# Performance work log

Measured on AMD Instinct MI355X. Metric: run time of the kernel, lower is better.

Reference implementation:

```python
import jax, jax.numpy as jnp
import numpy as np

ACT_BITS = 8
W_BITS = 8
BN_EPS = 1e-5


def _round_ste(x):
    # straight-through round (HAWQ-style ste_round)
    return x + jax.lax.stop_gradient(jnp.round(x) - x)


def _quant_sym(x, bits):
    # symmetric per-tensor fake quantization; scale treated as constant (EMA min/max in original)
    n = float(2 ** (bits - 1) - 1)
    s = jax.lax.stop_gradient(jnp.maximum(jnp.max(jnp.abs(x)) / n, 1e-8))
    xq = jnp.clip(_round_ste(x / s), -n - 1.0, n) * s
    return xq, s


def _conv(x, w, stride, pad):
    return jax.lax.conv_general_dilated(
        x, w, (stride, stride), [(pad, pad), (pad, pad)],
        dimension_numbers=("NCHW", "OIHW", "NCHW"))


def _quant_bn(x, gamma, beta, mean, var):
    # fold BN into a per-channel scale+bias; quantize the folded scale like a weight
    ws = gamma * jax.lax.rsqrt(var + BN_EPS)          # [C]
    wq, ws_scale = _quant_sym(ws, W_BITS)
    b = beta - mean * wq                               # [C]
    return x * wq[None, :, None, None] + b[None, :, None, None], ws_scale


def setup_inputs() -> dict:
    key = jax.random.key(0)
    ks = jax.random.split(key, 16)
    d = {}
    d["x"] = jax.random.normal(ks[0], (32, 128, 56, 56), jnp.float32)
    d["w1"] = jax.random.normal(ks[1], (256, 128, 3, 3), jnp.float32) * 0.05
    d["w2"] = jax.random.normal(ks[2], (256, 256, 3, 3), jnp.float32) * 0.05
    d["w_id"] = jax.random.normal(ks[3], (256, 128, 1, 1), jnp.float32) * 0.05
    for i, pfx in enumerate(["bn1", "bn2", "id"]):
        k4 = jax.random.split(ks[4 + i], 4)
        d[pfx + "_gamma"] = jax.random.uniform(k4[0], (256,), jnp.float32) + 0.5
        d[pfx + "_beta"] = jax.random.normal(k4[1], (256,), jnp.float32) * 0.1
        d[pfx + "_mean"] = jax.random.normal(k4[2], (256,), jnp.float32) * 0.1
        d[pfx + "_var"] = jax.random.uniform(k4[3], (256,), jnp.float32) + 0.5
    return d


def reference(x, w1, w2, w_id,
              bn1_gamma, bn1_beta, bn1_mean, bn1_var,
              bn2_gamma, bn2_beta, bn2_mean, bn2_var,
              id_gamma, id_beta, id_mean, id_var):
    # quant_act on block input
    xq, act_s = _quant_sym(x, ACT_BITS)

    # identity branch: 1x1 stride-2 quantized conv -> quant_act -> folded quant bn
    w_id_q, _ = _quant_sym(w_id, W_BITS)
    identity = _conv(xq, w_id_q, 2, 0)
    identity, _ = _quant_sym(identity, ACT_BITS)
    identity, _ = _quant_bn(identity, id_gamma, id_beta, id_mean, id_var)

    # main branch conv1 (3x3 stride 2) -> act quant -> bn -> relu -> act quant
    w1_q, _ = _quant_sym(w1, W_BITS)
    h = _conv(xq, w1_q, 2, 1)
    h, _ = _quant_sym(h, ACT_BITS)
    h, _ = _quant_bn(h, bn1_gamma, bn1_beta, bn1_mean, bn1_var)
    h = jax.nn.relu(h)
    h, _ = _quant_sym(h, ACT_BITS)

    # conv2 (3x3 stride 1) -> act quant -> bn
    w2_q, _ = _quant_sym(w2, W_BITS)
    h = _conv(h, w2_q, 1, 1)
    h, _ = _quant_sym(h, ACT_BITS)
    h, _ = _quant_bn(h, bn2_gamma, bn2_beta, bn2_mean, bn2_var)

    # residual add -> int32 requant -> relu
    h = h + identity
    h, out_s = _quant_sym(h, ACT_BITS)
    h = jax.nn.relu(h)
    return h, out_s
```

## Files before the change

### kernel.cpp

```cpp
#include <hip/hip_runtime.h>
#include <limits.h>

#define THREADS 256
#define GRID_BLOCKS 896

typedef int vi4 __attribute__((ext_vector_type(4)));

__device__ __forceinline__ float clamp8f(float q) { return fminf(fmaxf(q, -128.0f), 127.0f); }
__device__ __forceinline__ float sc_from_bits(unsigned b) {
  return fmaxf(__uint_as_float(b) / 127.0f, 1e-8f);
}
__device__ __forceinline__ signed char q8(float v, float s) {
  return (signed char)(int)clamp8f(rintf(v / s));
}


__device__ __forceinline__ void gbar(int* IS, int base, int bx) {
  asm volatile("s_waitcnt vmcnt(0)" ::: "memory");
  int old = __hip_atomic_fetch_add(IS + base + (bx & 7) * 16, 1, __ATOMIC_RELAXED,
                                   __HIP_MEMORY_SCOPE_AGENT);
  if (old == 111) {
    int r = __hip_atomic_fetch_add(IS + base + 128, 1, __ATOMIC_RELAXED, __HIP_MEMORY_SCOPE_AGENT);
    if (r == 7)
      __hip_atomic_fetch_add(IS + base + 144, 1, __ATOMIC_RELAXED, __HIP_MEMORY_SCOPE_AGENT);
  }
  while (__hip_atomic_load(IS + base + 144, __ATOMIC_RELAXED, __HIP_MEMORY_SCOPE_SYSTEM) == 0)
    __builtin_amdgcn_s_sleep(2);
}

__device__ __forceinline__ void amax_body(const float4* __restrict__ p, int n4, int bid,
                                          int nblocks, int* __restrict__ slot) {
  const int tid = threadIdx.x;
  const int stride = nblocks * THREADS;
  float m = 0.0f;
  int i = bid * THREADS + tid;
  for (; i + 3 * stride < n4; i += 4 * stride) {
    float4 v0 = p[i];
    float4 v1 = p[i + stride];
    float4 v2 = p[i + 2 * stride];
    float4 v3 = p[i + 3 * stride];
    float m0 = fmaxf(fmaxf(fabsf(v0.x), fabsf(v0.y)), fmaxf(fabsf(v0.z), fabsf(v0.w)));
    float m1 = fmaxf(fmaxf(fabsf(v1.x), fabsf(v1.y)), fmaxf(fabsf(v1.z), fabsf(v1.w)));
    float m2 = fmaxf(fmaxf(fabsf(v2.x), fabsf(v2.y)), fmaxf(fabsf(v2.z), fabsf(v2.w)));
    float m3 = fmaxf(fmaxf(fabsf(v3.x), fabsf(v3.y)), fmaxf(fabsf(v3.z), fabsf(v3.w)));
    m = fmaxf(m, fmaxf(fmaxf(m0, m1), fmaxf(m2, m3)));
  }
  for (; i < n4; i += stride) {
    float4 v = p[i];
    m = fmaxf(m, fmaxf(fmaxf(fabsf(v.x), fabsf(v.y)), fmaxf(fabsf(v.z), fabsf(v.w))));
  }
#pragma unroll
  for (int k = 32; k >= 1; k >>= 1) m = fmaxf(m, __shfl_xor(m, k));
  __shared__ float wred[4];
  if ((tid & 63) == 0) wred[tid >> 6] = m;
  __syncthreads();
  if (tid == 0) {
    m = fmaxf(fmaxf(wred[0], wred[1]), fmaxf(wred[2], wred[3]));
    atomicMax(slot, __float_as_int(m));
  }
}

__global__ __launch_bounds__(THREADS) void k_pre(
    int* IS, const float* g1, const float* be1, const float* m1, const float* v1, float* wq1,
    float* b1, const float* g2, const float* be2, const float* m2, const float* v2, float* wq2,
    float* b2, const float* gi, const float* bei, const float* mi, const float* vvi, float* wqi,
    float* bi, const float4* w1, const float4* w2, const float4* wid, const float4* x) {
  int b = blockIdx.x;
  int c = threadIdx.x;
  if (b < 3) {
    if (b == 0) {
      IS[128 + c] = 0;
      IS[384 + c] = 0;
      IS[640 + c] = 0;
      if (c < 192) IS[896 + c] = 0;
    }
    const float *gamma, *beta, *mean, *var;
    float *wq, *bb;
    if (b == 0) { gamma = g1; beta = be1; mean = m1; var = v1; wq = wq1; bb = b1; }
    else if (b == 1) { gamma = g2; beta = be2; mean = m2; var = v2; wq = wq2; bb = b2; }
    else { gamma = gi; beta = bei; mean = mi; var = vvi; wq = wqi; bb = bi; }
    __shared__ float red[THREADS];
    float ws = gamma[c] * (1.0f / sqrtf(var[c] + 1e-5f));
    red[c] = fabsf(ws);
    __syncthreads();
    for (int s = THREADS / 2; s > 0; s >>= 1) {
      if (c < s) red[c] = fmaxf(red[c], red[c + s]);
      __syncthreads();
    }
    float sws = fmaxf(red[0] / 127.0f, 1e-8f);
    float q = clamp8f(rintf(ws / sws)) * sws;
    wq[c] = q;
    bb[c] = beta[c] - mean[c] * q;
    return;
  }
  b -= 3;
  if (b < 64) { amax_body(w1, 73728, b, 64, IS + 1); return; }
  b -= 64;
  if (b < 128) { amax_body(w2, 147456, b, 128, IS + 2); return; }
  b -= 128;
  if (b < 16) { amax_body(wid, 8192, b, 16, IS + 3); return; }
  b -= 16;
  amax_body(x, 3211264, b, 512, IS + 0);
}

__global__ __launch_bounds__(THREADS) void k_quant(const float* __restrict__ x,
                                                   int* __restrict__ X8,
                                                   const float* __restrict__ w1f,
                                                   vi4* __restrict__ W1m,
                                                   const float* __restrict__ w2f,
                                                   vi4* __restrict__ W2m,
                                                   const float* __restrict__ widf,
                                                   vi4* __restrict__ Widm,
                                                   const unsigned* __restrict__ ISu) {
  __shared__ signed char tile[56 * 132];
  int b = blockIdx.x;
  int t = threadIdx.x;
  if (b < 1792) {
    float s = sc_from_bits(ISu[0]);
    int h = b % 56, n = b / 56;
    const float* xp = x + ((n * 128) * 56 + h) * 56;
#pragma unroll
    for (int k = 0; k < 28; ++k) {
      int i = t + k * 256;
      int w = i % 56, c = i / 56;
      tile[w * 132 + c] = q8(xp[c * 3136 + w], s);
    }
    __syncthreads();
    int* op = X8 + (n * 56 + h) * 56 * 32;
#pragma unroll
    for (int k = 0; k < 7; ++k) {
      int i = t + k * 256;
      int w = i >> 5, c4 = (i & 31) * 4;
      const signed char* tp = tile + w * 132 + c4;
      op[i] = (int)(unsigned char)tp[0] | ((int)(unsigned char)tp[1] << 8) |
              ((int)(unsigned char)tp[2] << 16) | ((int)(unsigned char)tp[3] << 24);
    }
    return;
  }
  if (b < 1864) {
    int tt = (b - 1792) * THREADS + t;
    float s = sc_from_bits(ISu[1]);
    int lane = tt & 63;
    int cotile = (tt >> 6) & 15;
    int ks = tt >> 10;
    int tap = ks >> 1, kc = ks & 1;
    int kh = tap / 3, kw = tap % 3;
    int co = cotile * 16 + (lane & 15);
    int ci0 = kc * 64 + (lane >> 4) * 16;
    const float* src = w1f + (co * 128 + ci0) * 9 + kh * 3 + kw;
    int r[4];
#pragma unroll
    for (int q = 0; q < 4; ++q) {
      unsigned b0 = (unsigned char)q8(src[(q * 4 + 0) * 9], s);
      unsigned b1 = (unsigned char)q8(src[(q * 4 + 1) * 9], s);
      unsigned b2 = (unsigned char)q8(src[(q * 4 + 2) * 9], s);
      unsigned b3 = (unsigned char)q8(src[(q * 4 + 3) * 9], s);
      r[q] = (int)(b0 | (b1 << 8) | (b2 << 16) | (b3 << 24));
    }
    vi4 v = {r[0], r[1], r[2], r[3]};
    W1m[tt] = v;
    return;
  }
  if (b < 2008) {
    int tt = (b - 1864) * THREADS + t;
    float s = sc_from_bits(ISu[2]);
    int lane = tt & 63;
    int cotile = (tt >> 6) & 15;
    int ks = tt >> 10;
    int tap = ks >> 2, kc = ks & 3;
    int kh = tap / 3, kw = tap % 3;
    int co = cotile * 16 + (lane & 15);
    int ci0 = kc * 64 + (lane >> 4) * 16;
    const float* src = w2f + (co * 256 + ci0) * 9 + kh * 3 + kw;
    int r[4];
#pragma unroll
    for (int q = 0; q < 4; ++q) {
      unsigned b0 = (unsigned char)q8(src[(q * 4 + 0) * 9], s);
      unsigned b1 = (unsigned char)q8(src[(q * 4 + 1) * 9], s);
      unsigned b2 = (unsigned char)q8(src[(q * 4 + 2) * 9], s);
      unsigned b3 = (unsigned char)q8(src[(q * 4 + 3) * 9], s);
      r[q] = (int)(b0 | (b1 << 8) | (b2 << 16) | (b3 << 24));
    }
    vi4 v = {r[0], r[1], r[2], r[3]};
    W2m[tt] = v;
    return;
  }
  {
    int tt = (b - 2008) * THREADS + t;
    float s = sc_from_bits(ISu[3]);
    int lane = tt & 63;
    int cotile = (tt >> 6) & 15;
    int ks = tt >> 10;
    int co = cotile * 16 + (lane & 15);
    int ci0 = ks * 64 + (lane >> 4) * 16;
    const float* src = widf + co * 128 + ci0;
    int r[4];
#pragma unroll
    for (int q = 0; q < 4; ++q) {
      unsigned b0 = (unsigned char)q8(src[q * 4 + 0], s);
      unsigned b1 = (unsigned char)q8(src[q * 4 + 1], s);
      unsigned b2 = (unsigned char)q8(src[q * 4 + 2], s);
      unsigned b3 = (unsigned char)q8(src[q * 4 + 3], s);
      r[q] = (int)(b0 | (b1 << 8) | (b2 << 16) | (b3 << 24));
    }
    vi4 v = {r[0], r[1], r[2], r[3]};
    Widm[tt] = v;
  }
}

#define MFMA_I8(a, b, c) __builtin_amdgcn_mfma_i32_16x16x64_i8(a, b, c, 0, 0, 0)

__device__ __forceinline__ signed char qact(int v, float sxw, float s_h1, float s_y2, float wq,
                                            float bb) {
  float hf = (float)v * sxw;
  float q = clamp8f(rintf(hf / s_h1));
  float hv = q * s_h1;
  float y = fmaxf(hv * wq + bb, 0.0f);
  float a = fminf(fmaxf(rintf(y / s_y2), -128.0f), 127.0f);
  return (signed char)(int)a;
}

__device__ __forceinline__ float sc_slot(const int* IS, int slot) {
  unsigned u = (unsigned)__hip_atomic_load((int*)(IS + slot), __ATOMIC_RELAXED,
                                           __HIP_MEMORY_SCOPE_AGENT);
  return fmaxf(__uint_as_float(u) / 127.0f, 1e-8f);
}

struct SumParams {
  float sxw2, s_h2, sxwid, s_idq;
};
__device__ __forceinline__ float sum_val(int v2, int vi, const SumParams& P, float wq2c, float b2c,
                                         float wqidc, float bidc) {
  float q2 = clamp8f(rintf((float)v2 * P.sxw2 / P.s_h2));
  float z = (q2 * P.s_h2) * wq2c + b2c;
  float qi = clamp8f(rintf((float)vi * P.sxwid / P.s_idq));
  float zi = (qi * P.s_idq) * wqidc + bidc;
  return z + zi;
}

__global__ __launch_bounds__(THREADS, 4) void k_ct(
    const int* X8, const vi4* __restrict__ W1m, const vi4* __restrict__ Widm,
    const vi4* __restrict__ W2m, int* A2p, int* IS, const float* __restrict__ wq1,
    const float* __restrict__ b1, const float* __restrict__ wq2, const float* __restrict__ b2,
    const float* __restrict__ wqid, const float* __restrict__ bidp, float* __restrict__ out,
    int* maxS2, int* minS2) {
  __shared__ __align__(16) int lds[9280];
  __shared__ int redA[4], redH[4];
  __shared__ int sVmax, sVmin;
  __shared__ float redF[4];
  __shared__ float sSxw, sSh1, sSy2, sSxwid, sSidq, sSxw2;
  __shared__ int sMh2;
  __shared__ float sOutS;
  const int tid = threadIdx.x;
  const int bx = blockIdx.x;
  const int n = bx / 28, rr = bx % 28;
  const int hp = rr >> 1, nh = rr & 1;
  const int ho0 = hp * 2;
  vi4 zero = {0, 0, 0, 0};

  for (int r = 0; r < 5; ++r) {
    int h = 2 * ho0 - 1 + r;
    int* dst = lds + r * 58 * 32;
    if (h >= 0 && h < 56) {
      const vi4* src = (const vi4*)(X8 + (n * 56 + h) * 56 * 32);
      for (int i4 = tid; i4 < 448; i4 += THREADS) {
        int col = i4 >> 3, e0 = (i4 & 7) * 4;
        int cell = r * 58 + col + 1;
        *(vi4*)(lds + cell * 32 + (e0 ^ ((cell & 7) << 2))) = src[i4];
      }
      if (tid < 32) dst[tid] = 0;
      else if (tid >= 128 && tid < 160) dst[57 * 32 + (tid - 128)] = 0;
    } else {
      for (int i4 = tid; i4 < 464; i4 += THREADS) ((vi4*)dst)[i4] = zero;
    }
  }
  __syncthreads();

  const int lane = tid & 63, wv = tid >> 6;
  const int mw = wv & 1, nw = wv >> 1;
  const int lm = lane & 15, quad = lane >> 4;
  const int woc0 = lm, woc1 = (16 + lm) > 27 ? 27 : (16 + lm);
  const int choff = quad * 4;
  const int ctbase = nh * 8 + nw * 4;

#define LDA(row, colp, sub)                                                              \
  (*(const vi4*)(lds + ((row) * 58 + (colp)) * 32 +                                      \
                 ((sub) ^ ((((row) * 58 + (colp)) & 7) << 2))))

  vi4 acc[2][4];
  vi4 accI[2][4];
  vi4 bA[4], bB[4];
  vi4 a0A, a1A, a0B, a1B;

#pragma unroll
  for (int mt = 0; mt < 2; ++mt)
#pragma unroll
    for (int ct = 0; ct < 4; ++ct) accI[mt][ct] = zero;
  const vi4* wibase = Widm + ctbase * 64 + lane;
  {
    const int row = 2 * mw + 1;
#pragma unroll
    for (int kc = 0; kc < 2; ++kc) {
      vi4 a0 = LDA(row, 2 * woc0 + 1, kc * 16 + choff);
      vi4 a1 = LDA(row, 2 * woc1 + 1, kc * 16 + choff);
#pragma unroll
      for (int ct = 0; ct < 4; ++ct) {
        vi4 b = wibase[kc * 1024 + ct * 64];
        accI[0][ct] = MFMA_I8(a0, b, accI[0][ct]);
        accI[1][ct] = MFMA_I8(a1, b, accI[1][ct]);
      }
    }
  }
  int am = 0;
#pragma unroll
  for (int ct = 0; ct < 4; ++ct)
#pragma unroll
    for (int mt = 0; mt < 2; ++mt)
#pragma unroll
      for (int r = 0; r < 4; ++r) {
        int wo = mt * 16 + quad * 4 + r;
        if (wo < 28) {
          int v = accI[mt][ct][r];
          am = max(am, v < 0 ? -v : v);
        }
      }
#pragma unroll
  for (int k = 32; k >= 1; k >>= 1) am = max(am, __shfl_xor(am, k));
  if (lane == 0) redA[wv] = am;

#pragma unroll
  for (int mt = 0; mt < 2; ++mt)
#pragma unroll
    for (int ct = 0; ct < 4; ++ct) acc[mt][ct] = zero;
  const vi4* wbase = W1m + ctbase * 64 + lane;
#pragma unroll
  for (int ct = 0; ct < 4; ++ct) bA[ct] = wbase[ct * 64];
  {
    a0A = LDA(2 * mw, 2 * woc0, choff);
    a1A = LDA(2 * mw, 2 * woc1, choff);
  }
#pragma unroll 1
  for (int ks = 0; ks < 18; ks += 2) {
    {
      const int ksn = ks + 1;
      const int khn = (ksn >= 6) + (ksn >= 12);
      const int t2 = ksn - khn * 6;
      const int kwn = t2 >> 1, kcn = t2 & 1;
#pragma unroll
      for (int ct = 0; ct < 4; ++ct) bB[ct] = wbase[ksn * 1024 + ct * 64];
      const int row = 2 * mw + khn;
      a0B = LDA(row, 2 * woc0 + kwn, kcn * 16 + choff);
      a1B = LDA(row, 2 * woc1 + kwn, kcn * 16 + choff);
    }
#pragma unroll
    for (int ct = 0; ct < 4; ++ct) {
      acc[0][ct] = MFMA_I8(a0A, bA[ct], acc[0][ct]);
      acc[1][ct] = MFMA_I8(a1A, bA[ct], acc[1][ct]);
    }
    if (ks + 2 < 18) {
      const int ksn = ks + 2;
      const int khn = (ksn >= 6) + (ksn >= 12);
      const int t2 = ksn - khn * 6;
      const int kwn = t2 >> 1, kcn = t2 & 1;
#pragma unroll
      for (int ct = 0; ct < 4; ++ct) bA[ct] = wbase[ksn * 1024 + ct * 64];
      const int row = 2 * mw + khn;
      a0A = LDA(row, 2 * woc0 + kwn, kcn * 16 + choff);
      a1A = LDA(row, 2 * woc1 + kwn, kcn * 16 + choff);
    }
#pragma unroll
    for (int ct = 0; ct < 4; ++ct) {
      acc[0][ct] = MFMA_I8(a0B, bB[ct], acc[0][ct]);
      acc[1][ct] = MFMA_I8(a1B, bB[ct], acc[1][ct]);
    }
  }
#undef LDA

#pragma unroll
  for (int ct = 0; ct < 4; ++ct) {
    int vmax = INT_MIN, vmin = INT_MAX;
#pragma unroll
    for (int mt = 0; mt < 2; ++mt)
#pragma unroll
      for (int r = 0; r < 4; ++r) {
        int wo = mt * 16 + quad * 4 + r;
        if (wo < 28) {
          int v = acc[mt][ct][r];
          vmax = max(vmax, v);
          vmin = min(vmin, v);
        }
      }
    vmax = max(vmax, __shfl_xor(vmax, 16));
    vmax = max(vmax, __shfl_xor(vmax, 32));
    vmin = min(vmin, __shfl_xor(vmin, 16));
    vmin = min(vmin, __shfl_xor(vmin, 32));
    if (lane < 16) {
      int cl = (nw * 4 + ct) * 16 + lane;
      __hip_atomic_store(maxS2 + bx * 256 + mw * 128 + cl, vmax, __ATOMIC_RELAXED,
                         __HIP_MEMORY_SCOPE_AGENT);
      __hip_atomic_store(minS2 + bx * 256 + mw * 128 + cl, vmin, __ATOMIC_RELAXED,
                         __HIP_MEMORY_SCOPE_AGENT);
    }
  }

  __syncthreads();
  if (tid == 0) {
    int a = max(max(redA[0], redA[1]), max(redA[2], redA[3]));
    atomicMax(IS + 5, a);
  }
#pragma unroll
  for (int ct = 0; ct < 4; ++ct) {
    const int cl = (nw * 4 + ct) * 16 + lm;
#pragma unroll
    for (int mt = 0; mt < 2; ++mt)
#pragma unroll
      for (int r = 0; r < 4; ++r) {
        int wo = mt * 16 + quad * 4 + r;
        if (wo < 28) lds[(mw * 28 + wo) * 130 + cl] = acc[mt][ct][r];
      }
  }
  __syncthreads();
  if (tid == 0) gbar(IS, 128, bx);
  __syncthreads();

  if (bx < 256) {
    const int c = bx, nhc = c >> 7, cl = c & 127;
    int vmax = INT_MIN, vmin = INT_MAX;
    for (int j = tid; j < 896; j += THREADS) {
      int bxx = nhc + ((j >> 1) << 1);
      int mwj = j & 1;
      int a = __hip_atomic_load(maxS2 + bxx * 256 + mwj * 128 + cl, __ATOMIC_RELAXED,
                                __HIP_MEMORY_SCOPE_AGENT);
      int i_ = __hip_atomic_load(minS2 + bxx * 256 + mwj * 128 + cl, __ATOMIC_RELAXED,
                                 __HIP_MEMORY_SCOPE_AGENT);
      vmax = max(vmax, a);
      vmin = min(vmin, i_);
    }
    int* rMax = lds + 7280;
    int* rMin = lds + 7536;
    rMax[tid] = vmax;
    rMin[tid] = vmin;
    __syncthreads();
    for (int s = 128; s > 0; s >>= 1) {
      if (tid < s) {
        rMax[tid] = max(rMax[tid], rMax[tid + s]);
        rMin[tid] = min(rMin[tid], rMin[tid + s]);
      }
      __syncthreads();
    }
    if (tid == 0) {
      sVmax = rMax[0];
      sVmin = rMin[0];
      int a1 = sVmax < 0 ? -sVmax : sVmax;
      int a0 = sVmin < 0 ? -sVmin : sVmin;
      atomicMax(IS + 4, max(a1, a0));
    }
  }
  __syncthreads();
  if (tid == 0) gbar(IS, 288, bx);
  __syncthreads();

  if (bx < 256 && tid == 0) {
    float sx = sc_slot(IS, 0);
    float sw1 = sc_slot(IS, 1);
    int mh1 = __hip_atomic_load(IS + 4, __ATOMIC_RELAXED, __HIP_MEMORY_SCOPE_AGENT);
    float sxw = sx * sw1;
    float s_h1 = fmaxf(sxw * (float)mh1 / 127.0f, 1e-8f);
    float wq = wq1[bx], bbc = b1[bx];
    float q1 = clamp8f(rintf((float)sVmax * sxw / s_h1));
    float q0 = clamp8f(rintf((float)sVmin * sxw / s_h1));
    float y1 = fmaxf(q1 * s_h1 * wq + bbc, 0.0f);
    float y0 = fmaxf(q0 * s_h1 * wq + bbc, 0.0f);
    atomicMax(IS + 7, __float_as_int(fmaxf(y1, y0)));
  }
  __syncthreads();
  if (tid == 0) gbar(IS, 448, bx);
  __syncthreads();

  if (tid == 0) {
    float sx = sc_slot(IS, 0);
    float sw1 = sc_slot(IS, 1);
    int mh1 = __hip_atomic_load(IS + 4, __ATOMIC_RELAXED, __HIP_MEMORY_SCOPE_AGENT);
    int mrf = __hip_atomic_load(IS + 7, __ATOMIC_RELAXED, __HIP_MEMORY_SCOPE_AGENT);
    float sxw = sx * sw1;
    sSxw = sxw;
    sSh1 = fmaxf(sxw * (float)mh1 / 127.0f, 1e-8f);
    float s_y2 = fmaxf(__int_as_float(mrf) / 127.0f, 1e-8f);
    sSy2 = s_y2;
    int mid = __hip_atomic_load(IS + 5, __ATOMIC_RELAXED, __HIP_MEMORY_SCOPE_AGENT);
    float swid = sc_slot(IS, 3);
    sSxwid = sx * swid;
    sSidq = fmaxf(sx * swid * (float)mid / 127.0f, 1e-8f);
    sSxw2 = s_y2 * sc_slot(IS, 2);
  }
  __syncthreads();

  {
    const float sxw = sSxw, s_h1 = sSh1, s_y2 = sSy2;
#pragma unroll
    for (int k = 0; k < 7; ++k) {
      int i = tid + k * 256;
      int sp = i >> 5, c4i = i & 31;
      int mwp = sp >= 28 ? 1 : 0;
      int wo = sp - mwp * 28;
      int c0 = nh * 128 + c4i * 4;
      const int* pk = lds + sp * 130 + c4i * 4;
      unsigned r0 = (unsigned char)qact(pk[0], sxw, s_h1, s_y2, wq1[c0], b1[c0]);
      unsigned r1 = (unsigned char)qact(pk[1], sxw, s_h1, s_y2, wq1[c0 + 1], b1[c0 + 1]);
      unsigned r2 = (unsigned char)qact(pk[2], sxw, s_h1, s_y2, wq1[c0 + 2], b1[c0 + 2]);
      unsigned r3 = (unsigned char)qact(pk[3], sxw, s_h1, s_y2, wq1[c0 + 3], b1[c0 + 3]);
      __hip_atomic_store(A2p + ((n * 28 + ho0 + mwp) * 28 + wo) * 64 + nh * 32 + c4i,
                         (int)(r0 | (r1 << 8) | (r2 << 16) | (r3 << 24)), __ATOMIC_RELAXED,
                         __HIP_MEMORY_SCOPE_AGENT);
    }
  }
  __syncthreads();
  if (tid == 0) gbar(IS, 608, bx);
  __syncthreads();

  for (int r = 0; r < 4; ++r) {
    int h = ho0 - 1 + r;
    int* dst = lds + r * 30 * 68;
    if (h >= 0 && h < 28) {
      const vi4* src = (const vi4*)(A2p + (n * 28 + h) * 28 * 64);
      for (int i4 = tid; i4 < 448; i4 += THREADS) {
        int col = i4 >> 4, c = (i4 & 15) * 4;
        *(vi4*)(dst + (col + 1) * 68 + c) = src[i4];
      }
      if (tid < 64) dst[tid] = 0;
      else if (tid >= 128 && tid < 192) dst[29 * 68 + (tid - 128)] = 0;
    } else {
      for (int i4 = tid; i4 < 510; i4 += THREADS) ((vi4*)dst)[i4] = zero;
    }
  }
  __syncthreads();

#pragma unroll
  for (int mt = 0; mt < 2; ++mt)
#pragma unroll
    for (int ct = 0; ct < 4; ++ct) acc[mt][ct] = zero;
  const vi4* wbase2 = W2m + ctbase * 64 + lane;
#pragma unroll
  for (int ct = 0; ct < 4; ++ct) bA[ct] = wbase2[ct * 64];
  {
    const int ro = mw * 30;
    a0A = *(const vi4*)(lds + (ro + woc0) * 68 + choff);
    a1A = *(const vi4*)(lds + (ro + woc1) * 68 + choff);
  }
#pragma unroll 1
  for (int ks = 0; ks < 36; ks += 2) {
    {
      const int ksn = ks + 1;
      const int khn = (ksn >= 12) + (ksn >= 24);
      const int t2 = ksn - khn * 12;
      const int kwn = t2 >> 2, kcn = t2 & 3;
#pragma unroll
      for (int ct = 0; ct < 4; ++ct) bB[ct] = wbase2[ksn * 1024 + ct * 64];
      const int ro = (mw + khn) * 30;
      a0B = *(const vi4*)(lds + (ro + woc0 + kwn) * 68 + kcn * 16 + choff);
      a1B = *(const vi4*)(lds + (ro + woc1 + kwn) * 68 + kcn * 16 + choff);
    }
#pragma unroll
    for (int ct = 0; ct < 4; ++ct) {
      acc[0][ct] = MFMA_I8(a0A, bA[ct], acc[0][ct]);
      acc[1][ct] = MFMA_I8(a1A, bA[ct], acc[1][ct]);
    }
    if (ks + 2 < 36) {
      const int ksn = ks + 2;
      const int khn = (ksn >= 12) + (ksn >= 24);
      const int t2 = ksn - khn * 12;
      const int kwn = t2 >> 2, kcn = t2 & 3;
#pragma unroll
      for (int ct = 0; ct < 4; ++ct) bA[ct] = wbase2[ksn * 1024 + ct * 64];
      const int ro = (mw + khn) * 30;
      a0A = *(const vi4*)(lds + (ro + woc0 + kwn) * 68 + kcn * 16 + choff);
      a1A = *(const vi4*)(lds + (ro + woc1 + kwn) * 68 + kcn * 16 + choff);
    }
#pragma unroll
    for (int ct = 0; ct < 4; ++ct) {
      acc[0][ct] = MFMA_I8(a0B, bB[ct], acc[0][ct]);
      acc[1][ct] = MFMA_I8(a1B, bB[ct], acc[1][ct]);
    }
  }

  int am2 = 0;
#pragma unroll
  for (int ct = 0; ct < 4; ++ct)
#pragma unroll
    for (int mt = 0; mt < 2; ++mt)
#pragma unroll
      for (int r = 0; r < 4; ++r) {
        int wo = mt * 16 + quad * 4 + r;
        if (wo < 28) {
          int v = acc[mt][ct][r];
          am2 = max(am2, v < 0 ? -v : v);
        }
      }
#pragma unroll
  for (int k = 32; k >= 1; k >>= 1) am2 = max(am2, __shfl_xor(am2, k));
  if (lane == 0) redH[wv] = am2;
  __syncthreads();
  if (tid == 0) {
    atomicMax(IS + 6, max(max(redH[0], redH[1]), max(redH[2], redH[3])));
    gbar(IS, 768, bx);
    sMh2 = __hip_atomic_load(IS + 6, __ATOMIC_RELAXED, __HIP_MEMORY_SCOPE_SYSTEM);
  }
  __syncthreads();

  SumParams P;
  P.sxw2 = sSxw2;
  P.s_h2 = fmaxf(sSxw2 * (float)sMh2 / 127.0f, 1e-8f);
  P.sxwid = sSxwid;
  P.s_idq = sSidq;

  float* sums = (float*)lds;
  float fm = 0.0f;
#pragma unroll
  for (int ct = 0; ct < 4; ++ct) {
    const int co = (ctbase + ct) * 16 + lm;
    const int cl = co - nh * 128;
    float w2c = wq2[co], b2c = b2[co], wic = wqid[co], bic = bidp[co];
#pragma unroll
    for (int mt = 0; mt < 2; ++mt)
#pragma unroll
      for (int r = 0; r < 4; ++r) {
        int wo = mt * 16 + quad * 4 + r;
        if (wo < 28) {
          int slot = cl * 57 + mw * 28 + wo;
          float sv = sum_val(acc[mt][ct][r], accI[mt][ct][r], P, w2c, b2c, wic, bic);
          sums[slot] = sv;
          fm = fmaxf(fm, fabsf(sv));
        }
      }
  }
#pragma unroll
  for (int k = 32; k >= 1; k >>= 1) fm = fmaxf(fm, __shfl_xor(fm, k));
  if (lane == 0) redF[wv] = fm;
  __syncthreads();
  if (tid == 0) {
    float a = fmaxf(fmaxf(redF[0], redF[1]), fmaxf(redF[2], redF[3]));
    atomicMax(IS + 11, __float_as_int(a));
    gbar(IS, 928, bx);
    int mb = __hip_atomic_load(IS + 11, __ATOMIC_RELAXED, __HIP_MEMORY_SCOPE_SYSTEM);
    sOutS = fmaxf(__int_as_float(mb) / 127.0f, 1e-8f);
  }
  __syncthreads();
  const float out_s = sOutS;

  float* ob = out + n * 200704 + (nh * 128) * 784 + ho0 * 28;
#pragma unroll
  for (int k = 0; k < 28; ++k) {
    int idx = tid + k * 256;
    int cl = idx / 56, rem = idx % 56;
    float sv = sums[cl * 57 + rem];
    float q = clamp8f(rintf(sv / out_s));
    ob[cl * 784 + rem] = q > 0.0f ? q * out_s : 0.0f;
  }
  if (bx == 0 && tid == 0) out[6422528] = out_s;
}

extern "C" void kernel_launch(void* const* d_in, const int* in_sizes, int n_in, void* d_out,
                              int out_size, void* d_ws, size_t ws_size, hipStream_t stream) {
  (void)in_sizes; (void)n_in; (void)out_size; (void)ws_size;
  const float* x = (const float*)d_in[0];
  const float* w1 = (const float*)d_in[1];
  const float* w2 = (const float*)d_in[2];
  const float* wid = (const float*)d_in[3];
  const float* bn1g = (const float*)d_in[4];
  const float* bn1b = (const float*)d_in[5];
  const float* bn1m = (const float*)d_in[6];
  const float* bn1v = (const float*)d_in[7];
  const float* bn2g = (const float*)d_in[8];
  const float* bn2b = (const float*)d_in[9];
  const float* bn2m = (const float*)d_in[10];
  const float* bn2v = (const float*)d_in[11];
  const float* idg = (const float*)d_in[12];
  const float* idb = (const float*)d_in[13];
  const float* idm = (const float*)d_in[14];
  const float* idv = (const float*)d_in[15];

  char* ws = (char*)d_ws;
  int* IS = (int*)ws;
  unsigned* ISu = (unsigned*)ws;
  float* wq1 = (float*)(ws + 4608);
  float* b1 = (float*)(ws + 5632);
  float* wq2 = (float*)(ws + 6656);
  float* b2 = (float*)(ws + 7680);
  float* wqid = (float*)(ws + 8704);
  float* bid = (float*)(ws + 9728);
  char* X8 = ws + 16384;
  char* W1m = X8 + 12845056;
  char* W2m = W1m + 294912;
  char* Widm = W2m + 589824;
  int* A2p = (int*)(Widm + 32768);
  float* out = (float*)d_out;
  int* maxS2 = (int*)d_out;
  int* minS2 = maxS2 + 896 * 256;

  k_pre<<<723, THREADS, 0, stream>>>(IS, bn1g, bn1b, bn1m, bn1v, wq1, b1, bn2g, bn2b, bn2m, bn2v,
                                     wq2, b2, idg, idb, idm, idv, wqid, bid, (const float4*)w1,
                                     (const float4*)w2, (const float4*)wid, (const float4*)x);
  k_quant<<<2016, THREADS, 0, stream>>>(x, (int*)X8, w1, (vi4*)W1m, w2, (vi4*)W2m, wid,
                                        (vi4*)Widm, ISu);
  k_ct<<<GRID_BLOCKS, THREADS, 0, stream>>>((const int*)X8, (const vi4*)W1m, (const vi4*)Widm,
                                            (const vi4*)W2m, A2p, IS, wq1, b1, wq2, b2, wqid, bid,
                                            out, maxS2, minS2);
}
```

Before: 238.7 us.

## Fuse input and weight quantization into persistent conv kernel behind a grid barrier

Removes the separate k_quant launch and performs x and weight int8 quantization/repacking at the start of the persistent conv kernel. Each of the 896 blocks quantizes two input rows and 64 weight vectors, then a new grid barrier is added before conv1, and all barrier slots are shifted. This saves one kernel launch and its tail at the cost of an extra grid-wide barrier and less parallelism for the quantization phase. Stores use relaxed atomics so other blocks can see the data after the barrier.

```diff
diff --git a/kernel.cpp b/kernel.cpp
--- a/kernel.cpp
+++ b/kernel.cpp
@@ -72,7 +72,8 @@
       IS[128 + c] = 0;
       IS[384 + c] = 0;
       IS[640 + c] = 0;
-      if (c < 192) IS[896 + c] = 0;
+      IS[896 + c] = 0;
+      if (c < 96) IS[1152 + c] = 0;
     }
     const float *gamma, *beta, *mean, *var;
     float *wq, *bb;
@@ -103,111 +104,6 @@
   amax_body(x, 3211264, b, 512, IS + 0);
 }
 
-__global__ __launch_bounds__(THREADS) void k_quant(const float* __restrict__ x,
-                                                   int* __restrict__ X8,
-                                                   const float* __restrict__ w1f,
-                                                   vi4* __restrict__ W1m,
-                                                   const float* __restrict__ w2f,
-                                                   vi4* __restrict__ W2m,
-                                                   const float* __restrict__ widf,
-                                                   vi4* __restrict__ Widm,
-                                                   const unsigned* __restrict__ ISu) {
-  __shared__ signed char tile[56 * 132];
-  int b = blockIdx.x;
-  int t = threadIdx.x;
-  if (b < 1792) {
-    float s = sc_from_bits(ISu[0]);
-    int h = b % 56, n = b / 56;
-    const float* xp = x + ((n * 128) * 56 + h) * 56;
-#pragma unroll
-    for (int k = 0; k < 28; ++k) {
-      int i = t + k * 256;
-      int w = i % 56, c = i / 56;
-      tile[w * 132 + c] = q8(xp[c * 3136 + w], s);
-    }
-    __syncthreads();
-    int* op = X8 + (n * 56 + h) * 56 * 32;
-#pragma unroll
-    for (int k = 0; k < 7; ++k) {
-      int i = t + k * 256;
-      int w = i >> 5, c4 = (i & 31) * 4;
-      const signed char* tp = tile + w * 132 + c4;
-      op[i] = (int)(unsigned char)tp[0] | ((int)(unsigned char)tp[1] << 8) |
-              ((int)(unsigned char)tp[2] << 16) | ((int)(unsigned char)tp[3] << 24);
-    }
-    return;
-  }
-  if (b < 1864) {
-    int tt = (b - 1792) * THREADS + t;
-    float s = sc_from_bits(ISu[1]);
-    int lane = tt & 63;
-    int cotile = (tt >> 6) & 15;
-    int ks = tt >> 10;
-    int tap = ks >> 1, kc = ks & 1;
-    int kh = tap / 3, kw = tap % 3;
-    int co = cotile * 16 + (lane & 15);
-    int ci0 = kc * 64 + (lane >> 4) * 16;
-    const float* src = w1f + (co * 128 + ci0) * 9 + kh * 3 + kw;
-    int r[4];
-#pragma unroll
-    for (int q = 0; q < 4; ++q) {
-      unsigned b0 = (unsigned char)q8(src[(q * 4 + 0) * 9], s);
-      unsigned b1 = (unsigned char)q8(src[(q * 4 + 1) * 9], s);
-      unsigned b2 = (unsigned char)q8(src[(q * 4 + 2) * 9], s);
-      unsigned b3 = (unsigned char)q8(src[(q * 4 + 3) * 9], s);
-      r[q] = (int)(b0 | (b1 << 8) | (b2 << 16) | (b3 << 24));
-    }
-    vi4 v = {r[0], r[1], r[2], r[3]};
-    W1m[tt] = v;
-    return;
-  }
-  if (b < 2008) {
-    int tt = (b - 1864) * THREADS + t;
-    float s = sc_from_bits(ISu[2]);
-    int lane = tt & 63;
-    int cotile = (tt >> 6) & 15;
-    int ks = tt >> 10;
-    int tap = ks >> 2, kc = ks & 3;
-    int kh = tap / 3, kw = tap % 3;
-    int co = cotile * 16 + (lane & 15);
-    int ci0 = kc * 64 + (lane >> 4) * 16;
-    const float* src = w2f + (co * 256 + ci0) * 9 + kh * 3 + kw;
-    int r[4];
-#pragma unroll
-    for (int q = 0; q < 4; ++q) {
-      unsigned b0 = (unsigned char)q8(src[(q * 4 + 0) * 9], s);
-      unsigned b1 = (unsigned char)q8(src[(q * 4 + 1) * 9], s);
-      unsigned b2 = (unsigned char)q8(src[(q * 4 + 2) * 9], s);
-      unsigned b3 = (unsigned char)q8(src[(q * 4 + 3) * 9], s);
-      r[q] = (int)(b0 | (b1 << 8) | (b2 << 16) | (b3 << 24));
-    }
-    vi4 v = {r[0], r[1], r[2], r[3]};
-    W2m[tt] = v;
-    return;
-  }
-  {
-    int tt = (b - 2008) * THREADS + t;
-    float s = sc_from_bits(ISu[3]);
-    int lane = tt & 63;
-    int cotile = (tt >> 6) & 15;
-    int ks = tt >> 10;
-    int co = cotile * 16 + (lane & 15);
-    int ci0 = ks * 64 + (lane >> 4) * 16;
-    const float* src = widf + co * 128 + ci0;
-    int r[4];
-#pragma unroll
-    for (int q = 0; q < 4; ++q) {
-      unsigned b0 = (unsigned char)q8(src[q * 4 + 0], s);
-      unsigned b1 = (unsigned char)q8(src[q * 4 + 1], s);
-      unsigned b2 = (unsigned char)q8(src[q * 4 + 2], s);
-      unsigned b3 = (unsigned char)q8(src[q * 4 + 3], s);
-      r[q] = (int)(b0 | (b1 << 8) | (b2 << 16) | (b3 << 24));
-    }
-    vi4 v = {r[0], r[1], r[2], r[3]};
-    Widm[tt] = v;
-  }
-}
-
 #define MFMA_I8(a, b, c) __builtin_amdgcn_mfma_i32_16x16x64_i8(a, b, c, 0, 0, 0)
 
 __device__ __forceinline__ signed char qact(int v, float sxw, float s_h1, float s_y2, float wq,
@@ -224,6 +120,16 @@
   unsigned u = (unsigned)__hip_atomic_load((int*)(IS + slot), __ATOMIC_RELAXED,
                                            __HIP_MEMORY_SCOPE_AGENT);
   return fmaxf(__uint_as_float(u) / 127.0f, 1e-8f);
+}
+
+__device__ __forceinline__ void st_w16(vi4* dst, int r0, int r1, int r2, int r3) {
+  unsigned long long lo = (unsigned long long)(unsigned)r0 |
+                          ((unsigned long long)(unsigned)r1 << 32);
+  unsigned long long hi = (unsigned long long)(unsigned)r2 |
+                          ((unsigned long long)(unsigned)r3 << 32);
+  unsigned long long* p = (unsigned long long*)dst;
+  __hip_atomic_store(p, lo, __ATOMIC_RELAXED, __HIP_MEMORY_SCOPE_AGENT);
+  __hip_atomic_store(p + 1, hi, __ATOMIC_RELAXED, __HIP_MEMORY_SCOPE_AGENT);
 }
 
 struct SumParams {
@@ -238,12 +144,12 @@
   return z + zi;
 }
 
-__global__ __launch_bounds__(THREADS, 4) void k_ct(
-    const int* X8, const vi4* __restrict__ W1m, const vi4* __restrict__ Widm,
-    const vi4* __restrict__ W2m, int* A2p, int* IS, const float* __restrict__ wq1,
-    const float* __restrict__ b1, const float* __restrict__ wq2, const float* __restrict__ b2,
-    const float* __restrict__ wqid, const float* __restrict__ bidp, float* __restrict__ out,
-    int* maxS2, int* minS2) {
+__global__ __launch_bounds__(THREADS, 4) void k_ct2(
+    const float* __restrict__ x, const float* __restrict__ w1f, const float* __restrict__ w2f,
+    const float* __restrict__ widf, int* X8, vi4* W1m, vi4* Widm, vi4* W2m, int* A2p, int* IS,
+    const float* __restrict__ wq1, const float* __restrict__ b1, const float* __restrict__ wq2,
+    const float* __restrict__ b2, const float* __restrict__ wqid, const float* __restrict__ bidp,
+    float* __restrict__ out, int* maxS2, int* minS2) {
   __shared__ __align__(16) int lds[9280];
   __shared__ int redA[4], redH[4];
   __shared__ int sVmax, sVmin;
@@ -257,12 +163,110 @@
   const int hp = rr >> 1, nh = rr & 1;
   const int ho0 = hp * 2;
   vi4 zero = {0, 0, 0, 0};
+  const unsigned* ISu = (const unsigned*)IS;
+
+  {
+    if (tid < 64) {
+      int g = bx * 64 + tid;
+      if (g < 18432) {
+        int tt = g;
+        float s = sc_from_bits(ISu[1]);
+        int lane2 = tt & 63;
+        int cotile = (tt >> 6) & 15;
+        int ks = tt >> 10;
+        int tap = ks >> 1, kc = ks & 1;
+        int kh = tap / 3, kw = tap % 3;
+        int co = cotile * 16 + (lane2 & 15);
+        int ci0 = kc * 64 + (lane2 >> 4) * 16;
+        const float* src = w1f + (co * 128 + ci0) * 9 + kh * 3 + kw;
+        int r[4];
+#pragma unroll
+        for (int q = 0; q < 4; ++q) {
+          unsigned b0 = (unsigned char)q8(src[(q * 4 + 0) * 9], s);
+          unsigned b1v = (unsigned char)q8(src[(q * 4 + 1) * 9], s);
+          unsigned b2v = (unsigned char)q8(src[(q * 4 + 2) * 9], s);
+          unsigned b3 = (unsigned char)q8(src[(q * 4 + 3) * 9], s);
+          r[q] = (int)(b0 | (b1v << 8) | (b2v << 16) | (b3 << 24));
+        }
+        st_w16(&W1m[tt], r[0], r[1], r[2], r[3]);
+      } else if (g < 55296) {
+        int tt = g - 18432;
+        float s = sc_from_bits(ISu[2]);
+        int lane2 = tt & 63;
+        int cotile = (tt >> 6) & 15;
+        int ks = tt >> 10;
+        int tap = ks >> 2, kc = ks & 3;
+        int kh = tap / 3, kw = tap % 3;
+        int co = cotile * 16 + (lane2 & 15);
+        int ci0 = kc * 64 + (lane2 >> 4) * 16;
+        const float* src = w2f + (co * 256 + ci0) * 9 + kh * 3 + kw;
+        int r[4];
+#pragma unroll
+        for (int q = 0; q < 4; ++q) {
+          unsigned b0 = (unsigned char)q8(src[(q * 4 + 0) * 9], s);
+          unsigned b1v = (unsigned char)q8(src[(q * 4 + 1) * 9], s);
+          unsigned b2v = (unsigned char)q8(src[(q * 4 + 2) * 9], s);
+          unsigned b3 = (unsigned char)q8(src[(q * 4 + 3) * 9], s);
+          r[q] = (int)(b0 | (b1v << 8) | (b2v << 16) | (b3 << 24));
+        }
+        st_w16(&W2m[tt], r[0], r[1], r[2], r[3]);
+      } else {
+        int tt = g - 55296;
+        float s = sc_from_bits(ISu[3]);
+        int lane2 = tt & 63;
+        int cotile = (tt >> 6) & 15;
+        int ks = tt >> 10;
+        int co = cotile * 16 + (lane2 & 15);
+        int ci0 = ks * 64 + (lane2 >> 4) * 16;
+        const float* src = widf + co * 128 + ci0;
+        int r[4];
+#pragma unroll
+        for (int q = 0; q < 4; ++q) {
+          unsigned b0 = (unsigned char)q8(src[q * 4 + 0], s);
+          unsigned b1v = (unsigned char)q8(src[q * 4 + 1], s);
+          unsigned b2v = (unsigned char)q8(src[q * 4 + 2], s);
+          unsigned b3 = (unsigned char)q8(src[q * 4 + 3], s);
+          r[q] = (int)(b0 | (b1v << 8) | (b2v << 16) | (b3 << 24));
+        }
+        st_w16(&Widm[tt], r[0], r[1], r[2], r[3]);
+      }
+    }
+    signed char* tile = (signed char*)lds;
+    const float sx = sc_from_bits(ISu[0]);
+#pragma unroll 1
+    for (int sl = 0; sl < 2; ++sl) {
+      int s = bx * 2 + sl;
+      int hq = s % 56, nq = s / 56;
+      const float* xp = x + ((nq * 128) * 56 + hq) * 56;
+#pragma unroll
+      for (int k = 0; k < 28; ++k) {
+        int i = tid + k * 256;
+        tile[(i % 56) * 132 + (i / 56)] = q8(xp[(i / 56) * 3136 + (i % 56)], sx);
+      }
+      __syncthreads();
+      int* op = X8 + (nq * 56 + hq) * 1792;
+#pragma unroll
+      for (int k = 0; k < 7; ++k) {
+        int i = tid + k * 256;
+        int w = i >> 5, c4 = (i & 31) * 4;
+        const signed char* tp = tile + w * 132 + c4;
+        __hip_atomic_store(op + i,
+                           (int)(unsigned char)tp[0] | ((int)(unsigned char)tp[1] << 8) |
+                               ((int)(unsigned char)tp[2] << 16) |
+                               ((int)(unsigned char)tp[3] << 24),
+                           __ATOMIC_RELAXED, __HIP_MEMORY_SCOPE_AGENT);
+      }
+      __syncthreads();
+    }
+  }
+  if (tid == 0) gbar(IS, 128, bx);
+  __syncthreads();
 
   for (int r = 0; r < 5; ++r) {
     int h = 2 * ho0 - 1 + r;
     int* dst = lds + r * 58 * 32;
     if (h >= 0 && h < 56) {
-      const vi4* src = (const vi4*)(X8 + (n * 56 + h) * 56 * 32);
+      const vi4* src = (const vi4*)(X8 + (n * 56 + h) * 1792);
       for (int i4 = tid; i4 < 448; i4 += THREADS) {
         int col = i4 >> 3, e0 = (i4 & 7) * 4;
         int cell = r * 58 + col + 1;
@@ -420,7 +424,7 @@
       }
   }
   __syncthreads();
-  if (tid == 0) gbar(IS, 128, bx);
+  if (tid == 0) gbar(IS, 288, bx);
   __syncthreads();
 
   if (bx < 256) {
@@ -457,7 +461,7 @@
     }
   }
   __syncthreads();
-  if (tid == 0) gbar(IS, 288, bx);
+  if (tid == 0) gbar(IS, 448, bx);
   __syncthreads();
 
   if (bx < 256 && tid == 0) {
@@ -474,7 +478,7 @@
     atomicMax(IS + 7, __float_as_int(fmaxf(y1, y0)));
   }
   __syncthreads();
-  if (tid == 0) gbar(IS, 448, bx);
+  if (tid == 0) gbar(IS, 608, bx);
   __syncthreads();
 
   if (tid == 0) {
@@ -515,7 +519,7 @@
     }
   }
   __syncthreads();
-  if (tid == 0) gbar(IS, 608, bx);
+  if (tid == 0) gbar(IS, 768, bx);
   __syncthreads();
 
   for (int r = 0; r < 4; ++r) {
@@ -602,7 +606,7 @@
   __syncthreads();
   if (tid == 0) {
     atomicMax(IS + 6, max(max(redH[0], redH[1]), max(redH[2], redH[3])));
-    gbar(IS, 768, bx);
+    gbar(IS, 928, bx);
     sMh2 = __hip_atomic_load(IS + 6, __ATOMIC_RELAXED, __HIP_MEMORY_SCOPE_SYSTEM);
   }
   __syncthreads();
@@ -640,7 +644,7 @@
   if (tid == 0) {
     float a = fmaxf(fmaxf(redF[0], redF[1]), fmaxf(redF[2], redF[3]));
     atomicMax(IS + 11, __float_as_int(a));
-    gbar(IS, 928, bx);
+    gbar(IS, 1088, bx);
     int mb = __hip_atomic_load(IS + 11, __ATOMIC_RELAXED, __HIP_MEMORY_SCOPE_SYSTEM);
     sOutS = fmaxf(__int_as_float(mb) / 127.0f, 1e-8f);
   }
@@ -681,13 +685,12 @@
 
   char* ws = (char*)d_ws;
   int* IS = (int*)ws;
-  unsigned* ISu = (unsigned*)ws;
-  float* wq1 = (float*)(ws + 4608);
-  float* b1 = (float*)(ws + 5632);
-  float* wq2 = (float*)(ws + 6656);
-  float* b2 = (float*)(ws + 7680);
-  float* wqid = (float*)(ws + 8704);
-  float* bid = (float*)(ws + 9728);
+  float* wq1 = (float*)(ws + 5120);
+  float* b1 = (float*)(ws + 6144);
+  float* wq2 = (float*)(ws + 7168);
+  float* b2 = (float*)(ws + 8192);
+  float* wqid = (float*)(ws + 9216);
+  float* bid = (float*)(ws + 10240);
   char* X8 = ws + 16384;
   char* W1m = X8 + 12845056;
   char* W2m = W1m + 294912;
@@ -700,9 +703,7 @@
   k_pre<<<723, THREADS, 0, stream>>>(IS, bn1g, bn1b, bn1m, bn1v, wq1, b1, bn2g, bn2b, bn2m, bn2v,
                                      wq2, b2, idg, idb, idm, idv, wqid, bid, (const float4*)w1,
                                      (const float4*)w2, (const float4*)wid, (const float4*)x);
-  k_quant<<<2016, THREADS, 0, stream>>>(x, (int*)X8, w1, (vi4*)W1m, w2, (vi4*)W2m, wid,
-                                        (vi4*)Widm, ISu);
-  k_ct<<<GRID_BLOCKS, THREADS, 0, stream>>>((const int*)X8, (const vi4*)W1m, (const vi4*)Widm,
-                                            (const vi4*)W2m, A2p, IS, wq1, b1, wq2, b2, wqid, bid,
-                                            out, maxS2, minS2);
-}
+  k_ct2<<<GRID_BLOCKS, THREADS, 0, stream>>>(x, w1, w2, wid, (int*)X8, (vi4*)W1m, (vi4*)Widm,
+                                             (vi4*)W2m, A2p, IS, wq1, b1, wq2, b2, wqid, bid, out,
+                                             maxS2, minS2);
+}
```

New measurement: 269.7 us. +13.0%, slower.
